# Optimization experiments

Measured on AMD Instinct MI355X. Metric: run time of the kernel, lower is better.

The kernel has to match this reference:

```python
import jax, jax.numpy as jnp
import numpy as np

N = 100000  # num nodes


def _gcn_conv(x, src, dst, W, b, n_nodes):
    """PyG GCNConv: symmetric normalization with implicit self-loops.
    out = D^{-1/2} (A + I) D^{-1/2} (x W) + b, deg counts in-edges + self-loop.
    """
    h = x @ W  # [N, H]
    ones = jnp.ones(src.shape[0], dtype=x.dtype)
    deg = jax.ops.segment_sum(ones, dst, num_segments=n_nodes) + 1.0  # +1 self-loop
    dinv = jax.lax.rsqrt(deg)  # [N]
    norm = dinv[src] * dinv[dst]  # [E]
    msg = h[src] * norm[:, None]  # gather + scale: memory-bound
    agg = jax.ops.segment_sum(msg, dst, num_segments=n_nodes)
    agg = agg + h * (dinv * dinv)[:, None]  # self-loop contribution
    return agg + b


def setup_inputs() -> dict:
    key = jax.random.key(0)
    k1, k2, k3, k4 = jax.random.split(key, 4)
    F = 64
    E = 1600000
    x = jax.random.normal(k1, (N, F), dtype=jnp.float32)
    edge_index = jax.random.randint(k2, (2, E), 0, N, dtype=jnp.int64)
    W1 = jax.random.normal(k3, (F, F), dtype=jnp.float32) / jnp.sqrt(jnp.float32(F))
    b1 = jnp.zeros((F,), dtype=jnp.float32)
    W2 = jax.random.normal(k4, (F, F), dtype=jnp.float32) / jnp.sqrt(jnp.float32(F))
    b2 = jnp.zeros((F,), dtype=jnp.float32)
    return {"x": x, "edge_index": edge_index, "W1": W1, "b1": b1, "W2": W2, "b2": b2}


def reference(x, edge_index, W1, b1, W2, b2):
    src, dst = edge_index[0], edge_index[1]
    h = _gcn_conv(x, src, dst, W1, b1, N)
    h = jax.nn.relu(h)
    # dropout(p=0.1) is identity in eval mode
    h = _gcn_conv(h, src, dst, W2, b2, N)
    return jax.nn.relu(h)
```

## Files before the change

kernel.cpp:

```cpp
#include <hip/hip_runtime.h>
#include <hip/hip_bf16.h>
#include <stdint.h>

#define NN 100000
#define NE 1600000
#define NBLK 256
#define EPB (NE / NBLK)
#define NBINS 782
#define NCELL (NBINS * NBLK)
#define NSB ((NCELL + 1023) / 1024)
#define GEMMB 782
#define BINCAP 4096


__device__ __forceinline__ unsigned pack_bf16(float a, float b) {
    unsigned ua = __float_as_uint(a);
    unsigned ub = __float_as_uint(b);
    ua += 0x7FFFu + ((ua >> 16) & 1u);
    ub += 0x7FFFu + ((ub >> 16) & 1u);
    return (ua >> 16) | (ub & 0xFFFF0000u);
}
#define BF_LO(u) __uint_as_float((u) << 16)
#define BF_HI(u) __uint_as_float((u) & 0xFFFF0000u)


__device__ __forceinline__ int ei_is64(const int* __restrict__ ei) {
    int z = 0;
#pragma unroll
    for (int i = 0; i < 16; ++i) z |= ei[2 * i + 1];
    return z == 0;
}


__global__ void __launch_bounds__(1024) k_hist(const int* __restrict__ ei,
                                               int* __restrict__ gcount) {
    __shared__ int lbin[NBINS];
    int t = threadIdx.x, blk = blockIdx.x;
    for (int i = t; i < NBINS; i += 1024) lbin[i] = 0;
    __syncthreads();
    int is64 = ei_is64(ei);
    int e0 = blk * EPB;
    if (is64) {
        const int2* p = (const int2*)ei;
        for (int e = e0 + t; e < e0 + EPB; e += 1024)
            atomicAdd(&lbin[p[NE + e].x >> 7], 1);
    } else {
        for (int e = e0 + t; e < e0 + EPB; e += 1024)
            atomicAdd(&lbin[ei[NE + e] >> 7], 1);
    }
    __syncthreads();
    for (int b = t; b < NBINS; b += 1024) gcount[b * NBLK + blk] = lbin[b];
}

__global__ void k_pscan1(const int* __restrict__ g, int* __restrict__ bsum) {
    __shared__ int sh[256];
    int t = threadIdx.x;
    int base = blockIdx.x * 1024 + t * 4;
    int s = 0;
#pragma unroll
    for (int j = 0; j < 4; ++j) { int i = base + j; if (i < NCELL) s += g[i]; }
    sh[t] = s; __syncthreads();
    for (int off = 128; off > 0; off >>= 1) {
        if (t < off) sh[t] += sh[t + off];
        __syncthreads();
    }
    if (t == 0) bsum[blockIdx.x] = sh[0];
}

__global__ void k_pscan23(const int* __restrict__ g, const int* __restrict__ bsum,
                          int* __restrict__ goff) {
    __shared__ int sh[256];
    __shared__ int boffs;
    int t = threadIdx.x;
    int bv = (t < NSB) ? bsum[t] : 0;
    sh[t] = bv; __syncthreads();
    for (int off = 1; off < 256; off <<= 1) {
        int tmp = (t >= off) ? sh[t - off] : 0;
        __syncthreads();
        sh[t] += tmp;
        __syncthreads();
    }
    if (t == blockIdx.x) boffs = sh[t] - bv;
    __syncthreads();
    int base = blockIdx.x * 1024 + t * 4;
    int v[4]; int s = 0;
#pragma unroll
    for (int j = 0; j < 4; ++j) { int i = base + j; v[j] = (i < NCELL) ? g[i] : 0; s += v[j]; }
    __syncthreads();
    sh[t] = s; __syncthreads();
    for (int off = 1; off < 256; off <<= 1) {
        int tmp = (t >= off) ? sh[t - off] : 0;
        __syncthreads();
        sh[t] += tmp;
        __syncthreads();
    }
    int run = sh[t] - s + boffs;
#pragma unroll
    for (int j = 0; j < 4; ++j) {
        int i = base + j;
        if (i < NCELL) { goff[i] = run; run += v[j]; }
    }
}

__global__ void __launch_bounds__(1024) k_scatter(const int* __restrict__ ei,
                                                  const int* __restrict__ goff,
                                                  unsigned* __restrict__ tmp) {
    __shared__ int lcur[NBINS];
    int t = threadIdx.x, blk = blockIdx.x;
    for (int i = t; i < NBINS; i += 1024) lcur[i] = 0;
    __syncthreads();
    int is64 = ei_is64(ei);
    int e0 = blk * EPB;
    for (int e = e0 + t; e < e0 + EPB; e += 1024) {
        int s, d;
        if (is64) {
            s = ((const int2*)ei)[e].x;
            d = ((const int2*)ei)[NE + e].x;
        } else {
            s = ei[e];
            d = ei[NE + e];
        }
        int b = d >> 7;
        int lr = atomicAdd(&lcur[b], 1);
        int pos = goff[b * NBLK + blk] + lr;
        tmp[pos] = (unsigned)s | ((unsigned)(d & 127) << 17);
    }
}


__device__ __forceinline__ void gemm_body(int gb, const float* __restrict__ X,
                                          const float* __restrict__ W,
                                          unsigned* __restrict__ Hb) {
    int wid = (gb * 256 + (int)threadIdx.x) >> 6;
    int lane = threadIdx.x & 63;
    int task = __builtin_amdgcn_readfirstlane(wid);
    const int ntasks = ((NN + 63) >> 6) * 2;
    if (task >= ntasks) return;
    int t = task >> 1;
    int ch = task & 1;
    int row = t * 64 + lane;
    int r = row < NN ? row : NN - 1;
    const float4* xp = (const float4*)(X + (size_t)r * 64);
    const float* Wb = W + ch * 32;
    float acc[32];
#pragma unroll
    for (int c = 0; c < 32; ++c) acc[c] = 0.f;
#pragma unroll 4
    for (int k4 = 0; k4 < 16; ++k4) {
        float4 xv = xp[k4];
#pragma unroll
        for (int kj = 0; kj < 4; ++kj) {
            float xk = (kj == 0) ? xv.x : (kj == 1) ? xv.y : (kj == 2) ? xv.z : xv.w;
            const float4* wr = (const float4*)(Wb + (k4 * 4 + kj) * 64);
#pragma unroll
            for (int c4 = 0; c4 < 8; ++c4) {
                float4 wv = wr[c4];
                acc[c4 * 4 + 0] += xk * wv.x;
                acc[c4 * 4 + 1] += xk * wv.y;
                acc[c4 * 4 + 2] += xk * wv.z;
                acc[c4 * 4 + 3] += xk * wv.w;
            }
        }
    }
    uint4* op = (uint4*)(Hb + (size_t)r * 32 + ch * 16);
#pragma unroll
    for (int q = 0; q < 4; ++q) {
        uint4 o;
        o.x = pack_bf16(acc[q * 8 + 0], acc[q * 8 + 1]);
        o.y = pack_bf16(acc[q * 8 + 2], acc[q * 8 + 3]);
        o.z = pack_bf16(acc[q * 8 + 4], acc[q * 8 + 5]);
        o.w = pack_bf16(acc[q * 8 + 6], acc[q * 8 + 7]);
        op[q] = o;
    }
}

__global__ void __launch_bounds__(256) k_gemm(const float* __restrict__ X,
                                              const float* __restrict__ W,
                                              unsigned* __restrict__ Hb) {
    gemm_body(blockIdx.x, X, W, Hb);
}


__global__ void __launch_bounds__(256) k_degcsr_gemm(const unsigned* __restrict__ tmp,
                                                     const int* __restrict__ goff,
                                                     int* __restrict__ rs,
                                                     float* __restrict__ dinv,
                                                     unsigned* __restrict__ csr,
                                                     const float* __restrict__ X,
                                                     const float* __restrict__ W1,
                                                     unsigned* __restrict__ Hb) {
    if (blockIdx.x >= NBINS) {
        gemm_body((int)blockIdx.x - NBINS, X, W1, Hb);
        return;
    }
    __shared__ unsigned cache[BINCAP];
    __shared__ int hist[128];
    __shared__ int cur[128];
    __shared__ int base_sh[128];
    int b = blockIdx.x, t = threadIdx.x;
    if (t < 128) { hist[t] = 0; cur[t] = 0; }
    __syncthreads();
    int bs = goff[b * NBLK];
    int be = (b == NBINS - 1) ? NE : goff[(b + 1) * NBLK];
    for (int e = bs + t; e < be; e += 256) {
        unsigned v = tmp[e];
        int i = e - bs;
        if (i < BINCAP) cache[i] = v;
        atomicAdd(&hist[v >> 17], 1);
    }
    __syncthreads();
    if (t < 128) {
        int node = b * 128 + t;
        if (node < NN) {
            int c = hist[t];
            int loff = 0;
            for (int i = 0; i < t; ++i) loff += hist[i];
            rs[node] = bs + loff;
            base_sh[t] = bs + loff;
            dinv[node] = rsqrtf((float)c + 1.0f);
        } else base_sh[t] = 0;
    }
    if (b == 0 && t == 0) rs[NN] = NE;
    __syncthreads();
    int cnt = be - bs;
    for (int i = t; i < cnt; i += 256) {
        unsigned v = (i < BINCAP) ? cache[i] : tmp[bs + i];
        int dl = v >> 17;
        int lr = atomicAdd(&cur[dl], 1);
        csr[base_sh[dl] + lr] = v & 0x1FFFFu;
    }
}


#define EDGE_ACC(wt, r)                                                       \
    {                                                                         \
        a0 += BF_LO((r).x) * (wt); a1 += BF_HI((r).x) * (wt);                 \
        a2 += BF_LO((r).y) * (wt); a3 += BF_HI((r).y) * (wt);                 \
        a4 += BF_LO((r).z) * (wt); a5 += BF_HI((r).z) * (wt);                 \
        a6 += BF_LO((r).w) * (wt); a7 += BF_HI((r).w) * (wt);                 \
    }

__global__ void __launch_bounds__(256) k_agg(const uint4* __restrict__ hb,
                                             const int* __restrict__ rs,
                                             const unsigned* __restrict__ csr,
                                             const float* __restrict__ dinv,
                                             const float* __restrict__ bias,
                                             float4* __restrict__ out4) {
    int wid = (blockIdx.x * blockDim.x + threadIdx.x) >> 6;
    int lane = threadIdx.x & 63;
    int node = __builtin_amdgcn_readfirstlane(wid);
    if (node >= NN) return;
    int g = lane >> 3;
    int s = lane & 7;
    float dn = dinv[node];
    int e0 = rs[node], e1 = rs[node + 1];
    float a0 = 0.f, a1 = 0.f, a2 = 0.f, a3 = 0.f;
    float a4 = 0.f, a5 = 0.f, a6 = 0.f, a7 = 0.f;
    int e = e0 + g;
    unsigned p0 = csr[e];
    unsigned p1 = csr[e + 8];
    for (; e + 8 < e1; e += 16) {
        unsigned q0 = csr[e + 16];
        unsigned q1 = csr[e + 24];
        float w0 = dinv[p0];
        float w1 = dinv[p1];
        uint4 r0 = hb[(size_t)p0 * 8 + s];
        uint4 r1 = hb[(size_t)p1 * 8 + s];
        EDGE_ACC(w0, r0);
        EDGE_ACC(w1, r1);
        p0 = q0; p1 = q1;
    }
    if (e < e1) {
        float w0 = dinv[p0];
        uint4 r0 = hb[(size_t)p0 * 8 + s];
        EDGE_ACC(w0, r0);
    }
#pragma unroll
    for (int m = 8; m <= 32; m <<= 1) {
        a0 += __shfl_xor(a0, m); a1 += __shfl_xor(a1, m);
        a2 += __shfl_xor(a2, m); a3 += __shfl_xor(a3, m);
        a4 += __shfl_xor(a4, m); a5 += __shfl_xor(a5, m);
        a6 += __shfl_xor(a6, m); a7 += __shfl_xor(a7, m);
    }
    if (lane < 8) {
        uint4 r = hb[(size_t)node * 8 + s];
        const float4* bp = (const float4*)(bias + s * 8);
        float4 b0 = bp[0], b1v = bp[1];
        float4 o0, o1;
        o0.x = fmaxf((a0 + BF_LO(r.x) * dn) * dn + b0.x, 0.f);
        o0.y = fmaxf((a1 + BF_HI(r.x) * dn) * dn + b0.y, 0.f);
        o0.z = fmaxf((a2 + BF_LO(r.y) * dn) * dn + b0.z, 0.f);
        o0.w = fmaxf((a3 + BF_HI(r.y) * dn) * dn + b0.w, 0.f);
        o1.x = fmaxf((a4 + BF_LO(r.z) * dn) * dn + b1v.x, 0.f);
        o1.y = fmaxf((a5 + BF_HI(r.z) * dn) * dn + b1v.y, 0.f);
        o1.z = fmaxf((a6 + BF_LO(r.w) * dn) * dn + b1v.z, 0.f);
        o1.w = fmaxf((a7 + BF_HI(r.w) * dn) * dn + b1v.w, 0.f);
        out4[(size_t)node * 16 + s * 2] = o0;
        out4[(size_t)node * 16 + s * 2 + 1] = o1;
    }
}


extern "C" void kernel_launch(void* const* d_in, const int* in_sizes, int n_in,
                              void* d_out, int out_size, void* d_ws, size_t ws_size,
                              hipStream_t stream) {
    const float* x  = (const float*)d_in[0];
    const int* ei   = (const int*)d_in[1];
    const float* W1 = (const float*)d_in[2];
    const float* b1 = (const float*)d_in[3];
    const float* W2 = (const float*)d_in[4];
    const float* b2 = (const float*)d_in[5];

    char* ws = (char*)d_ws;
    size_t off = 0;
    auto alloc = [&](size_t bytes) -> char* {
        char* p = ws + off;
        off = (off + bytes + 511) & ~(size_t)511;
        return p;
    };
    int*      gcount= (int*)alloc((size_t)NCELL * 4);
    int*      goff  = (int*)alloc((size_t)NCELL * 4);
    int*      bsum  = (int*)alloc((size_t)NSB * 4);
    unsigned* tmp   = (unsigned*)alloc((size_t)NE * 4);
    unsigned* csr   = (unsigned*)alloc((size_t)NE * 4);
    int*      rs    = (int*)alloc((size_t)(NN + 1) * 4);
    float*    dinv  = (float*)alloc((size_t)NN * 4);
    unsigned* hbuf  = (unsigned*)alloc((size_t)NN * 32 * 4);
    float*    hmid  = (float*)d_out;

    k_hist<<<NBLK, 1024, 0, stream>>>(ei, gcount);
    k_pscan1<<<NSB, 256, 0, stream>>>(gcount, bsum);
    k_pscan23<<<NSB, 256, 0, stream>>>(gcount, bsum, goff);
    k_scatter<<<NBLK, 1024, 0, stream>>>(ei, goff, tmp);
    k_degcsr_gemm<<<NBINS + GEMMB, 256, 0, stream>>>(tmp, goff, rs, dinv, csr,
                                                     x, W1, hbuf);
    k_agg<<<(NN * 64) / 256, 256, 0, stream>>>((const uint4*)hbuf, rs, csr, dinv, b1,
                                               (float4*)hmid);
    k_gemm<<<GEMMB, 256, 0, stream>>>(hmid, W2, hbuf);
    k_agg<<<(NN * 64) / 256, 256, 0, stream>>>((const uint4*)hbuf, rs, csr, dinv, b2,
                                               (float4*)d_out);
}
```

Measured before the change: 248.8 us.

## Build CSR with global atomic degree count and atomic-cursor fill

Replaces the two-level binned counting sort (per-block histograms, large prefix scan, scatter into a temp array, per-bin local sort) with a direct global-atomic degree count, a scan over nodes, and an atomic-cursor fill of the CSR. This cuts a kernel launch, the temp buffer and a pass over the edges. In exchange it relies on heavy global atomics and leaves neighbour order within each row nondeterministic, which hurts gather locality and makes float sums order-dependent. The aggregation kernel also switches to 32-bit byte-offset address arithmetic for its gathers.

```diff
diff --git a/kernel.cpp b/kernel.cpp
--- a/kernel.cpp
+++ b/kernel.cpp
@@ -4,13 +4,9 @@
 
 #define NN 100000
 #define NE 1600000
-#define NBLK 256
-#define EPB (NE / NBLK)
-#define NBINS 782
-#define NCELL (NBINS * NBLK)
-#define NSB ((NCELL + 1023) / 1024)
+#define NSC 98
+#define FBLK 3125
 #define GEMMB 782
-#define BINCAP 4096
 
 
 __device__ __forceinline__ unsigned pack_bf16(float a, float b) {
@@ -32,33 +28,32 @@
 }
 
 
-__global__ void __launch_bounds__(1024) k_hist(const int* __restrict__ ei,
-                                               int* __restrict__ gcount) {
-    __shared__ int lbin[NBINS];
-    int t = threadIdx.x, blk = blockIdx.x;
-    for (int i = t; i < NBINS; i += 1024) lbin[i] = 0;
-    __syncthreads();
+__global__ void __launch_bounds__(256) k_deg(const int* __restrict__ ei,
+                                             int* __restrict__ deg) {
     int is64 = ei_is64(ei);
-    int e0 = blk * EPB;
+    int i = blockIdx.x * 256 + threadIdx.x;
+    int e = i * 2;
+    if (e >= NE) return;
+    int d0, d1;
     if (is64) {
         const int2* p = (const int2*)ei;
-        for (int e = e0 + t; e < e0 + EPB; e += 1024)
-            atomicAdd(&lbin[p[NE + e].x >> 7], 1);
+        d0 = p[NE + e].x;
+        d1 = p[NE + e + 1].x;
     } else {
-        for (int e = e0 + t; e < e0 + EPB; e += 1024)
-            atomicAdd(&lbin[ei[NE + e] >> 7], 1);
-    }
-    __syncthreads();
-    for (int b = t; b < NBINS; b += 1024) gcount[b * NBLK + blk] = lbin[b];
-}
-
-__global__ void k_pscan1(const int* __restrict__ g, int* __restrict__ bsum) {
+        int2 dd = ((const int2*)(ei + NE))[i];
+        d0 = dd.x; d1 = dd.y;
+    }
+    atomicAdd(&deg[d0], 1);
+    atomicAdd(&deg[d1], 1);
+}
+
+__global__ void k_scan1(const int* __restrict__ deg, int* __restrict__ bsum) {
     __shared__ int sh[256];
     int t = threadIdx.x;
     int base = blockIdx.x * 1024 + t * 4;
     int s = 0;
 #pragma unroll
-    for (int j = 0; j < 4; ++j) { int i = base + j; if (i < NCELL) s += g[i]; }
+    for (int j = 0; j < 4; ++j) { int i = base + j; if (i < NN) s += deg[i]; }
     sh[t] = s; __syncthreads();
     for (int off = 128; off > 0; off >>= 1) {
         if (t < off) sh[t] += sh[t + off];
@@ -67,12 +62,13 @@
     if (t == 0) bsum[blockIdx.x] = sh[0];
 }
 
-__global__ void k_pscan23(const int* __restrict__ g, const int* __restrict__ bsum,
-                          int* __restrict__ goff) {
+__global__ void k_scan2(const int* __restrict__ deg, const int* __restrict__ bsum,
+                        int* __restrict__ rs, int* __restrict__ cur,
+                        float* __restrict__ dinv) {
     __shared__ int sh[256];
     __shared__ int boffs;
     int t = threadIdx.x;
-    int bv = (t < NSB) ? bsum[t] : 0;
+    int bv = (t < NSC) ? bsum[t] : 0;
     sh[t] = bv; __syncthreads();
     for (int off = 1; off < 256; off <<= 1) {
         int tmp = (t >= off) ? sh[t - off] : 0;
@@ -85,7 +81,7 @@
     int base = blockIdx.x * 1024 + t * 4;
     int v[4]; int s = 0;
 #pragma unroll
-    for (int j = 0; j < 4; ++j) { int i = base + j; v[j] = (i < NCELL) ? g[i] : 0; s += v[j]; }
+    for (int j = 0; j < 4; ++j) { int i = base + j; v[j] = (i < NN) ? deg[i] : 0; s += v[j]; }
     __syncthreads();
     sh[t] = s; __syncthreads();
     for (int off = 1; off < 256; off <<= 1) {
@@ -98,33 +94,14 @@
 #pragma unroll
     for (int j = 0; j < 4; ++j) {
         int i = base + j;
-        if (i < NCELL) { goff[i] = run; run += v[j]; }
-    }
-}
-
-__global__ void __launch_bounds__(1024) k_scatter(const int* __restrict__ ei,
-                                                  const int* __restrict__ goff,
-                                                  unsigned* __restrict__ tmp) {
-    __shared__ int lcur[NBINS];
-    int t = threadIdx.x, blk = blockIdx.x;
-    for (int i = t; i < NBINS; i += 1024) lcur[i] = 0;
-    __syncthreads();
-    int is64 = ei_is64(ei);
-    int e0 = blk * EPB;
-    for (int e = e0 + t; e < e0 + EPB; e += 1024) {
-        int s, d;
-        if (is64) {
-            s = ((const int2*)ei)[e].x;
-            d = ((const int2*)ei)[NE + e].x;
-        } else {
-            s = ei[e];
-            d = ei[NE + e];
+        if (i < NN) {
+            rs[i] = run;
+            cur[i] = run;
+            dinv[i] = rsqrtf((float)v[j] + 1.0f);
+            run += v[j];
         }
-        int b = d >> 7;
-        int lr = atomicAdd(&lcur[b], 1);
-        int pos = goff[b * NBLK + blk] + lr;
-        tmp[pos] = (unsigned)s | ((unsigned)(d & 127) << 17);
-    }
+    }
+    if (blockIdx.x == 0 && t == 0) rs[NN] = NE;
 }
 
 
@@ -181,54 +158,34 @@
 }
 
 
-__global__ void __launch_bounds__(256) k_degcsr_gemm(const unsigned* __restrict__ tmp,
-                                                     const int* __restrict__ goff,
-                                                     int* __restrict__ rs,
-                                                     float* __restrict__ dinv,
-                                                     unsigned* __restrict__ csr,
-                                                     const float* __restrict__ X,
-                                                     const float* __restrict__ W1,
-                                                     unsigned* __restrict__ Hb) {
-    if (blockIdx.x >= NBINS) {
-        gemm_body((int)blockIdx.x - NBINS, X, W1, Hb);
+__global__ void __launch_bounds__(256) k_fillcsr_gemm(const int* __restrict__ ei,
+                                                      int* __restrict__ cur,
+                                                      unsigned* __restrict__ csr,
+                                                      const float* __restrict__ X,
+                                                      const float* __restrict__ W1,
+                                                      unsigned* __restrict__ Hb) {
+    if (blockIdx.x >= FBLK) {
+        gemm_body((int)blockIdx.x - FBLK, X, W1, Hb);
         return;
     }
-    __shared__ unsigned cache[BINCAP];
-    __shared__ int hist[128];
-    __shared__ int cur[128];
-    __shared__ int base_sh[128];
-    int b = blockIdx.x, t = threadIdx.x;
-    if (t < 128) { hist[t] = 0; cur[t] = 0; }
-    __syncthreads();
-    int bs = goff[b * NBLK];
-    int be = (b == NBINS - 1) ? NE : goff[(b + 1) * NBLK];
-    for (int e = bs + t; e < be; e += 256) {
-        unsigned v = tmp[e];
-        int i = e - bs;
-        if (i < BINCAP) cache[i] = v;
-        atomicAdd(&hist[v >> 17], 1);
-    }
-    __syncthreads();
-    if (t < 128) {
-        int node = b * 128 + t;
-        if (node < NN) {
-            int c = hist[t];
-            int loff = 0;
-            for (int i = 0; i < t; ++i) loff += hist[i];
-            rs[node] = bs + loff;
-            base_sh[t] = bs + loff;
-            dinv[node] = rsqrtf((float)c + 1.0f);
-        } else base_sh[t] = 0;
-    }
-    if (b == 0 && t == 0) rs[NN] = NE;
-    __syncthreads();
-    int cnt = be - bs;
-    for (int i = t; i < cnt; i += 256) {
-        unsigned v = (i < BINCAP) ? cache[i] : tmp[bs + i];
-        int dl = v >> 17;
-        int lr = atomicAdd(&cur[dl], 1);
-        csr[base_sh[dl] + lr] = v & 0x1FFFFu;
-    }
+    int is64 = ei_is64(ei);
+    int i = blockIdx.x * 256 + threadIdx.x;
+    int e = i * 2;
+    if (e >= NE) return;
+    int s0, s1, d0, d1;
+    if (is64) {
+        const int2* p = (const int2*)ei;
+        s0 = p[e].x;      s1 = p[e + 1].x;
+        d0 = p[NE + e].x; d1 = p[NE + e + 1].x;
+    } else {
+        int2 ss = ((const int2*)ei)[i];
+        int2 dd = ((const int2*)(ei + NE))[i];
+        s0 = ss.x; s1 = ss.y; d0 = dd.x; d1 = dd.y;
+    }
+    int p0 = atomicAdd(&cur[d0], 1);
+    csr[p0] = (unsigned)s0;
+    int p1 = atomicAdd(&cur[d1], 1);
+    csr[p1] = (unsigned)s1;
 }
 
 
@@ -252,6 +209,9 @@
     if (node >= NN) return;
     int g = lane >> 3;
     int s = lane & 7;
+    const char* hbc = (const char*)hb;
+    const char* dvc = (const char*)dinv;
+    unsigned soff = (unsigned)s << 4;
     float dn = dinv[node];
     int e0 = rs[node], e1 = rs[node + 1];
     float a0 = 0.f, a1 = 0.f, a2 = 0.f, a3 = 0.f;
@@ -262,17 +222,17 @@
     for (; e + 8 < e1; e += 16) {
         unsigned q0 = csr[e + 16];
         unsigned q1 = csr[e + 24];
-        float w0 = dinv[p0];
-        float w1 = dinv[p1];
-        uint4 r0 = hb[(size_t)p0 * 8 + s];
-        uint4 r1 = hb[(size_t)p1 * 8 + s];
+        float w0 = *(const float*)(dvc + (size_t)(p0 << 2));
+        float w1 = *(const float*)(dvc + (size_t)(p1 << 2));
+        uint4 r0 = *(const uint4*)(hbc + (size_t)((p0 << 7) + soff));
+        uint4 r1 = *(const uint4*)(hbc + (size_t)((p1 << 7) + soff));
         EDGE_ACC(w0, r0);
         EDGE_ACC(w1, r1);
         p0 = q0; p1 = q1;
     }
     if (e < e1) {
-        float w0 = dinv[p0];
-        uint4 r0 = hb[(size_t)p0 * 8 + s];
+        float w0 = *(const float*)(dvc + (size_t)(p0 << 2));
+        uint4 r0 = *(const uint4*)(hbc + (size_t)((p0 << 7) + soff));
         EDGE_ACC(w0, r0);
     }
 #pragma unroll
@@ -318,22 +278,20 @@
         off = (off + bytes + 511) & ~(size_t)511;
         return p;
     };
-    int*      gcount= (int*)alloc((size_t)NCELL * 4);
-    int*      goff  = (int*)alloc((size_t)NCELL * 4);
-    int*      bsum  = (int*)alloc((size_t)NSB * 4);
-    unsigned* tmp   = (unsigned*)alloc((size_t)NE * 4);
+    int*      deg   = (int*)alloc((size_t)NN * 4);
+    int*      bsum  = (int*)alloc((size_t)NSC * 4);
     unsigned* csr   = (unsigned*)alloc((size_t)NE * 4);
     int*      rs    = (int*)alloc((size_t)(NN + 1) * 4);
+    int*      cur   = (int*)alloc((size_t)NN * 4);
     float*    dinv  = (float*)alloc((size_t)NN * 4);
     unsigned* hbuf  = (unsigned*)alloc((size_t)NN * 32 * 4);
     float*    hmid  = (float*)d_out;
 
-    k_hist<<<NBLK, 1024, 0, stream>>>(ei, gcount);
-    k_pscan1<<<NSB, 256, 0, stream>>>(gcount, bsum);
-    k_pscan23<<<NSB, 256, 0, stream>>>(gcount, bsum, goff);
-    k_scatter<<<NBLK, 1024, 0, stream>>>(ei, goff, tmp);
-    k_degcsr_gemm<<<NBINS + GEMMB, 256, 0, stream>>>(tmp, goff, rs, dinv, csr,
-                                                     x, W1, hbuf);
+    hipMemsetAsync(deg, 0, (size_t)NN * 4, stream);
+    k_deg<<<FBLK, 256, 0, stream>>>(ei, deg);
+    k_scan1<<<NSC, 256, 0, stream>>>(deg, bsum);
+    k_scan2<<<NSC, 256, 0, stream>>>(deg, bsum, rs, cur, dinv);
+    k_fillcsr_gemm<<<FBLK + GEMMB, 256, 0, stream>>>(ei, cur, csr, x, W1, hbuf);
     k_agg<<<(NN * 64) / 256, 256, 0, stream>>>((const uint4*)hbuf, rs, csr, dinv, b1,
                                                (float4*)hmid);
     k_gemm<<<GEMMB, 256, 0, stream>>>(hmid, W2, hbuf);
```

Result: slower. 402.7 us (+61.9%).
